# Optimization experiments

Measured on AMD Instinct MI355X. Metric: run time of the kernel, lower is better.

## Reference

```python
import jax, jax.numpy as jnp
import numpy as np

NUM_USERS = 1_000_000
NUM_ITEMS = 1_000_000
MF_DIM = 16
MLP_DIM = 32
BATCH = 1_048_576


def setup_inputs() -> dict:
    key = jax.random.key(0)
    ks = jax.random.split(key, 12)
    s = 0.05
    return {
        "user": jax.random.randint(ks[0], (BATCH,), 0, NUM_USERS),
        "item": jax.random.randint(ks[1], (BATCH,), 0, NUM_ITEMS),
        "mf_user_tbl": jax.random.normal(ks[2], (NUM_USERS, MF_DIM), jnp.float32) * s,
        "mf_item_tbl": jax.random.normal(ks[3], (NUM_ITEMS, MF_DIM), jnp.float32) * s,
        "mlp_user_tbl": jax.random.normal(ks[4], (NUM_USERS, MLP_DIM), jnp.float32) * s,
        "mlp_item_tbl": jax.random.normal(ks[5], (NUM_ITEMS, MLP_DIM), jnp.float32) * s,
        "W1": jax.random.normal(ks[6], (2 * MLP_DIM, 64), jnp.float32) * s,  # [64,64]
        "b1": jnp.zeros((64,), jnp.float32),
        "W2": jax.random.normal(ks[7], (64, 32), jnp.float32) * s,
        "b2": jnp.zeros((32,), jnp.float32),
        "Wo": jax.random.normal(ks[8], (MF_DIM + 32, 1), jnp.float32) * s,
        "bo": jnp.zeros((1,), jnp.float32),
    }


def reference(user, item, mf_user_tbl, mf_item_tbl, mlp_user_tbl, mlp_item_tbl,
              W1, b1, W2, b2, Wo, bo):
    # GMF branch: elementwise product of user/item MF embeddings  [B, mf_dim]
    mf_out = mf_user_tbl[user] * mf_item_tbl[item]
    # MLP branch: concat embeddings -> Linear/ReLU x2
    mlp_in = jnp.concatenate([mlp_user_tbl[user], mlp_item_tbl[item]], axis=1)  # [B, 64]
    h = jax.nn.relu(mlp_in @ W1 + b1)   # [B, 64]
    h = jax.nn.relu(h @ W2 + b2)        # [B, 32]
    combined = jnp.concatenate([mf_out, h], axis=1)  # [B, 48]
    return combined @ Wo + bo           # [B, 1]
```

## Files before the change

### kernel.cpp

```cpp
#include <hip/hip_runtime.h>


typedef _Float16 half8 __attribute__((ext_vector_type(8)));
typedef float floatx4 __attribute__((ext_vector_type(4)));

#define WPB 4
#define TPW 4

__global__ __launch_bounds__(64) void build_frags(const float* __restrict__ W1,
                                                  const float* __restrict__ W2,
                                                  _Float16* __restrict__ wf) {
    const int l = threadIdx.x;
    const int c = l & 15, q = l >> 4;
    #pragma unroll
    for (int s = 0; s < 2; ++s)
        #pragma unroll
        for (int t = 0; t < 4; ++t) {
            _Float16* dst = wf + (size_t)((s * 4 + t) * 64 + l) * 8;
            #pragma unroll
            for (int j = 0; j < 8; ++j) {
                const int k = s * 32 + q * 8 + j;
                const int n = t * 16 + c;
                dst[j] = (_Float16)W1[k * 64 + n];
            }
        }
    _Float16* w2b = wf + 8 * 64 * 8;
    #pragma unroll
    for (int s = 0; s < 2; ++s)
        #pragma unroll
        for (int t = 0; t < 2; ++t) {
            _Float16* dst = w2b + (size_t)((s * 2 + t) * 64 + l) * 8;
            #pragma unroll
            for (int j = 0; j < 8; ++j) {
                const int k = s * 32 + q * 8 + j;
                const int n = t * 16 + c;
                dst[j] = (_Float16)W2[k * 32 + n];
            }
        }
}

__global__ __launch_bounds__(256) void neumf_mfma(
    const int* __restrict__ user, const int* __restrict__ item,
    const float* __restrict__ mfu, const float* __restrict__ mfi,
    const float* __restrict__ mlu, const float* __restrict__ mli,
    const _Float16* __restrict__ wf,
    const float* __restrict__ b1, const float* __restrict__ b2,
    const float* __restrict__ Wo, const float* __restrict__ bo,
    float* __restrict__ out, int n)
{
    __shared__ __align__(16) _Float16 x2s[WPB][16 * 72];
    __shared__ __align__(16) float    pss[WPB][16 * 20];

    const int lane = threadIdx.x & 63;
    const int w    = threadIdx.x >> 6;
    const int wave_id = blockIdx.x * WPB + w;
    const int c = lane & 15, q = lane >> 4;

    half8 w1f[2][4], w2f[2][2];
    #pragma unroll
    for (int s = 0; s < 2; ++s)
        #pragma unroll
        for (int t = 0; t < 4; ++t)
            w1f[s][t] = *(const half8*)(wf + (size_t)((s * 4 + t) * 64 + lane) * 8);
    const _Float16* w2b = wf + 8 * 64 * 8;
    #pragma unroll
    for (int s = 0; s < 2; ++s)
        #pragma unroll
        for (int t = 0; t < 2; ++t)
            w2f[s][t] = *(const half8*)(w2b + (size_t)((s * 2 + t) * 64 + lane) * 8);

    const float b1v0 = b1[c], b1v1 = b1[16 + c], b1v2 = b1[32 + c], b1v3 = b1[48 + c];
    const float b2v0 = b2[c], b2v1 = b2[16 + c];
    const float wo2v0 = Wo[16 + c], wo2v1 = Wo[32 + c];
    const float4 wo4 = *(const float4*)(Wo + q * 4);
    const float bov = bo[0];

    _Float16* x2 = x2s[w];
    float*    pb = pss[w];

    #pragma unroll 1
    for (int i = 0; i < TPW; ++i) {
        const int base = (wave_id * TPW + i) * 16;
        if (base >= n) break;
        int si = base + c; if (si >= n) si = n - 1;
        const int u  = user[si];
        const int it = item[si];

        const float4* pu = (const float4*)(mlu + (size_t)u  * 32 + q * 8);
        const float4* pi = (const float4*)(mli + (size_t)it * 32 + q * 8);
        const float4 ua = pu[0], ub = pu[1];
        const float4 ia = pi[0], ib = pi[1];
        const float4 gu = *(const float4*)(mfu + (size_t)u  * 16 + q * 4);
        const float4 gi = *(const float4*)(mfi + (size_t)it * 16 + q * 4);

        half8 au, ai;
        au[0] = (_Float16)ua.x; au[1] = (_Float16)ua.y; au[2] = (_Float16)ua.z; au[3] = (_Float16)ua.w;
        au[4] = (_Float16)ub.x; au[5] = (_Float16)ub.y; au[6] = (_Float16)ub.z; au[7] = (_Float16)ub.w;
        ai[0] = (_Float16)ia.x; ai[1] = (_Float16)ia.y; ai[2] = (_Float16)ia.z; ai[3] = (_Float16)ia.w;
        ai[4] = (_Float16)ib.x; ai[5] = (_Float16)ib.y; ai[6] = (_Float16)ib.z; ai[7] = (_Float16)ib.w;

        floatx4 a0 = {0.f,0.f,0.f,0.f}, a1 = {0.f,0.f,0.f,0.f};
        floatx4 a2 = {0.f,0.f,0.f,0.f}, a3 = {0.f,0.f,0.f,0.f};
        a0 = __builtin_amdgcn_mfma_f32_16x16x32_f16(au, w1f[0][0], a0, 0, 0, 0);
        a1 = __builtin_amdgcn_mfma_f32_16x16x32_f16(au, w1f[0][1], a1, 0, 0, 0);
        a2 = __builtin_amdgcn_mfma_f32_16x16x32_f16(au, w1f[0][2], a2, 0, 0, 0);
        a3 = __builtin_amdgcn_mfma_f32_16x16x32_f16(au, w1f[0][3], a3, 0, 0, 0);
        a0 = __builtin_amdgcn_mfma_f32_16x16x32_f16(ai, w1f[1][0], a0, 0, 0, 0);
        a1 = __builtin_amdgcn_mfma_f32_16x16x32_f16(ai, w1f[1][1], a1, 0, 0, 0);
        a2 = __builtin_amdgcn_mfma_f32_16x16x32_f16(ai, w1f[1][2], a2, 0, 0, 0);
        a3 = __builtin_amdgcn_mfma_f32_16x16x32_f16(ai, w1f[1][3], a3, 0, 0, 0);

        float p = gu.x * gi.x * wo4.x + gu.y * gi.y * wo4.y
                + gu.z * gi.z * wo4.z + gu.w * gi.w * wo4.w;
        p += __shfl_xor(p, 16);
        p += __shfl_xor(p, 32);

        #pragma unroll
        for (int r = 0; r < 4; ++r) {
            const int m = q * 4 + r;
            x2[m * 72 +  0 + c] = (_Float16)fmaxf(a0[r] + b1v0, 0.f);
            x2[m * 72 + 16 + c] = (_Float16)fmaxf(a1[r] + b1v1, 0.f);
            x2[m * 72 + 32 + c] = (_Float16)fmaxf(a2[r] + b1v2, 0.f);
            x2[m * 72 + 48 + c] = (_Float16)fmaxf(a3[r] + b1v3, 0.f);
        }

        const half8 h0 = *(const half8*)(x2 + c * 72 +  0 + q * 8);
        const half8 h1 = *(const half8*)(x2 + c * 72 + 32 + q * 8);
        floatx4 d0 = {0.f,0.f,0.f,0.f}, d1 = {0.f,0.f,0.f,0.f};
        d0 = __builtin_amdgcn_mfma_f32_16x16x32_f16(h0, w2f[0][0], d0, 0, 0, 0);
        d0 = __builtin_amdgcn_mfma_f32_16x16x32_f16(h1, w2f[1][0], d0, 0, 0, 0);
        d1 = __builtin_amdgcn_mfma_f32_16x16x32_f16(h0, w2f[0][1], d1, 0, 0, 0);
        d1 = __builtin_amdgcn_mfma_f32_16x16x32_f16(h1, w2f[1][1], d1, 0, 0, 0);

        #pragma unroll
        for (int r = 0; r < 4; ++r) {
            const float v = fmaxf(d0[r] + b2v0, 0.f) * wo2v0
                          + fmaxf(d1[r] + b2v1, 0.f) * wo2v1;
            pb[(q * 4 + r) * 20 + c] = v;
        }

        if (lane < 16) {
            const float4* row = (const float4*)(pb + lane * 20);
            const float4 r0 = row[0], r1 = row[1], r2 = row[2], r3 = row[3];
            const float s16 = (((r0.x + r0.y) + (r0.z + r0.w)) + ((r1.x + r1.y) + (r1.z + r1.w)))
                            + (((r2.x + r2.y) + (r2.z + r2.w)) + ((r3.x + r3.y) + (r3.z + r3.w)));
            if (base + lane < n)
                out[base + lane] = s16 + p + bov;
        }
    }
}

extern "C" void kernel_launch(void* const* d_in, const int* in_sizes, int n_in,
                              void* d_out, int out_size, void* d_ws, size_t ws_size,
                              hipStream_t stream) {
    const int*   user = (const int*)  d_in[0];
    const int*   item = (const int*)  d_in[1];
    const float* mfu  = (const float*)d_in[2];
    const float* mfi  = (const float*)d_in[3];
    const float* mlu  = (const float*)d_in[4];
    const float* mli  = (const float*)d_in[5];
    const float* W1   = (const float*)d_in[6];
    const float* b1   = (const float*)d_in[7];
    const float* W2   = (const float*)d_in[8];
    const float* b2   = (const float*)d_in[9];
    const float* Wo   = (const float*)d_in[10];
    const float* bo   = (const float*)d_in[11];
    float* out = (float*)d_out;
    _Float16* wf = (_Float16*)d_ws;

    build_frags<<<1, 64, 0, stream>>>(W1, W2, wf);

    const int n = in_sizes[0];
    const int tiles  = (n + 15) / 16;
    const int waves  = (tiles + TPW - 1) / TPW;
    const int blocks = (waves + WPB - 1) / WPB;
    neumf_mfma<<<blocks, 256, 0, stream>>>(user, item, mfu, mfi, mlu, mli,
                                           wf, b1, b2, Wo, bo, out, n);
}
```

Before: 373.4 us.

## Double-buffer embedding gathers across tiles and load indices once per wave

```diff
diff --git a/kernel.cpp b/kernel.cpp
--- a/kernel.cpp
+++ b/kernel.cpp
@@ -20,8 +20,8 @@
             #pragma unroll
             for (int j = 0; j < 8; ++j) {
                 const int k = s * 32 + q * 8 + j;
-                const int n = t * 16 + c;
-                dst[j] = (_Float16)W1[k * 64 + n];
+                const int nn = t * 16 + c;
+                dst[j] = (_Float16)W1[k * 64 + nn];
             }
         }
     _Float16* w2b = wf + 8 * 64 * 8;
@@ -33,8 +33,8 @@
             #pragma unroll
             for (int j = 0; j < 8; ++j) {
                 const int k = s * 32 + q * 8 + j;
-                const int n = t * 16 + c;
-                dst[j] = (_Float16)W2[k * 32 + n];
+                const int nn = t * 16 + c;
+                dst[j] = (_Float16)W2[k * 32 + nn];
             }
         }
 }
@@ -56,6 +56,9 @@
     const int wave_id = blockIdx.x * WPB + w;
     const int c = lane & 15, q = lane >> 4;
 
+    const int tb = wave_id * (TPW * 16);
+    if (tb >= n) return;
+
     half8 w1f[2][4], w2f[2][2];
     #pragma unroll
     for (int s = 0; s < 2; ++s)
@@ -78,26 +81,30 @@
     _Float16* x2 = x2s[w];
     float*    pb = pss[w];
 
-    #pragma unroll 1
-    for (int i = 0; i < TPW; ++i) {
-        const int base = (wave_id * TPW + i) * 16;
-        if (base >= n) break;
-        int si = base + c; if (si >= n) si = n - 1;
-        const int u  = user[si];
-        const int it = item[si];
-
-        const float4* pu = (const float4*)(mlu + (size_t)u  * 32 + q * 8);
-        const float4* pi = (const float4*)(mli + (size_t)it * 32 + q * 8);
-        const float4 ua = pu[0], ub = pu[1];
-        const float4 ia = pi[0], ib = pi[1];
-        const float4 gu = *(const float4*)(mfu + (size_t)u  * 16 + q * 4);
-        const float4 gi = *(const float4*)(mfi + (size_t)it * 16 + q * 4);
+    int gidx = tb + lane; if (gidx >= n) gidx = n - 1;
+    const int uAll  = user[gidx];
+    const int itAll = item[gidx];
+
+#define ISSUE(i, UA, UB, IA, IB, GU, GI) do {                                  \
+        const int u_ = __shfl(uAll,  (i) * 16 + c);                            \
+        const int v_ = __shfl(itAll, (i) * 16 + c);                            \
+        const float4* pu_ = (const float4*)(mlu + (size_t)u_ * 32 + q * 8);    \
+        UA = pu_[0]; UB = pu_[1];                                              \
+        const float4* pi_ = (const float4*)(mli + (size_t)v_ * 32 + q * 8);    \
+        IA = pi_[0]; IB = pi_[1];                                              \
+        GU = *(const float4*)(mfu + (size_t)u_ * 16 + q * 4);                  \
+        GI = *(const float4*)(mfi + (size_t)v_ * 16 + q * 4);                  \
+    } while (0)
+
+    auto compute = [&](int base, float4 ua, float4 ub, float4 iax, float4 ibx,
+                       float4 gu, float4 gi) {
+        if (base >= n) return;
 
         half8 au, ai;
-        au[0] = (_Float16)ua.x; au[1] = (_Float16)ua.y; au[2] = (_Float16)ua.z; au[3] = (_Float16)ua.w;
-        au[4] = (_Float16)ub.x; au[5] = (_Float16)ub.y; au[6] = (_Float16)ub.z; au[7] = (_Float16)ub.w;
-        ai[0] = (_Float16)ia.x; ai[1] = (_Float16)ia.y; ai[2] = (_Float16)ia.z; ai[3] = (_Float16)ia.w;
-        ai[4] = (_Float16)ib.x; ai[5] = (_Float16)ib.y; ai[6] = (_Float16)ib.z; ai[7] = (_Float16)ib.w;
+        au[0] = (_Float16)ua.x;  au[1] = (_Float16)ua.y;  au[2] = (_Float16)ua.z;  au[3] = (_Float16)ua.w;
+        au[4] = (_Float16)ub.x;  au[5] = (_Float16)ub.y;  au[6] = (_Float16)ub.z;  au[7] = (_Float16)ub.w;
+        ai[0] = (_Float16)iax.x; ai[1] = (_Float16)iax.y; ai[2] = (_Float16)iax.z; ai[3] = (_Float16)iax.w;
+        ai[4] = (_Float16)ibx.x; ai[5] = (_Float16)ibx.y; ai[6] = (_Float16)ibx.z; ai[7] = (_Float16)ibx.w;
 
         floatx4 a0 = {0.f,0.f,0.f,0.f}, a1 = {0.f,0.f,0.f,0.f};
         floatx4 a2 = {0.f,0.f,0.f,0.f}, a3 = {0.f,0.f,0.f,0.f};
@@ -147,7 +154,24 @@
             if (base + lane < n)
                 out[base + lane] = s16 + p + bov;
         }
-    }
+    };
+
+    float4 a_ua, a_ub, a_ia, a_ib, a_gu, a_gi;
+    float4 b_ua, b_ub, b_ia, b_ib, b_gu, b_gi;
+
+    ISSUE(0, a_ua, a_ub, a_ia, a_ib, a_gu, a_gi);
+    ISSUE(1, b_ua, b_ub, b_ia, b_ib, b_gu, b_gi);
+
+    compute(tb + 0 * 16, a_ua, a_ub, a_ia, a_ib, a_gu, a_gi);
+    ISSUE(2, a_ua, a_ub, a_ia, a_ib, a_gu, a_gi);
+
+    compute(tb + 1 * 16, b_ua, b_ub, b_ia, b_ib, b_gu, b_gi);
+    ISSUE(3, b_ua, b_ub, b_ia, b_ib, b_gu, b_gi);
+
+    compute(tb + 2 * 16, a_ua, a_ub, a_ia, a_ib, a_gu, a_gi);
+    compute(tb + 3 * 16, b_ua, b_ub, b_ia, b_ib, b_gu, b_gi);
+
+#undef ISSUE
 }
 
 extern "C" void kernel_launch(void* const* d_in, const int* in_sizes, int n_in,
```

Measured after the change: 369.0 us. No clear change (-1.2%).
